# Performance work log

Hardware: AMD Instinct MI355X
Metric: run time of the kernel (lower is better)

The kernel has to match this reference:

```python
import jax, jax.numpy as jnp
import numpy as np


def setup_inputs() -> dict:
    key = jax.random.key(0)
    ks = jax.random.split(key, 10)
    B, T, D = 256, 256, 256
    CH, L, K = 128, 3, 10          # chunk_size, levels, conv_size
    H = CH * L                     # hidden_dim = 384
    G = 4 * H + 2 * L              # gate projection width = 1542
    HS = H // 6

    def xavier(k, shape):
        fan_in, fan_out = shape[0], shape[-1]
        lim = np.sqrt(6.0 / (fan_in + fan_out)).astype(np.float32)
        return jax.random.uniform(k, shape, jnp.float32, -lim, lim)

    x = jax.random.normal(ks[0], (B, T, D), jnp.float32)
    lengths = jax.random.randint(ks[1], (B,), 1, T + 1).astype(jnp.int64)
    Wk = xavier(ks[2], (D + 1, G)); bk = jnp.zeros((G,), jnp.float32)
    Wr = xavier(ks[3], (H + 1, G)); br = jnp.zeros((G,), jnp.float32)
    Ws = xavier(ks[4], (H, HS));    bs = jnp.zeros((HS,), jnp.float32)
    Wrs = xavier(ks[5], (HS, H));   brs = jnp.zeros((H,), jnp.float32)
    Wc = xavier(ks[6], (H, H, K)) / np.sqrt(K)  # Conv1d weight (out, in, k)
    bc = jnp.zeros((H,), jnp.float32)
    return {"x": x, "lengths": lengths, "Wk": Wk, "bk": bk, "Wr": Wr,
            "br": br, "Ws": Ws, "bs": bs, "Wrs": Wrs, "brs": brs,
            "Wc": Wc, "bc": bc}


def _cumax_l2r(z):
    return jnp.cumsum(jax.nn.softmax(z, axis=-1), axis=-1)


def _cumax_r2l(z):
    zf = jnp.flip(z, -1)
    return jnp.flip(jnp.cumsum(jax.nn.softmax(zf, axis=-1), axis=-1), -1)


def reference(x, lengths, Wk, bk, Wr, br, Ws, bs, Wrs, brs, Wc, bc):
    B, T, D = x.shape
    H = Wr.shape[0] - 1
    G = Wk.shape[1]
    L = (G - 4 * H) // 2
    CH = H // L
    K = Wc.shape[2]
    ones = jnp.ones((B, 1), x.dtype)

    def step(carry, xt):
        c, h, tmp_h, tmp_dis = carry
        # two linear projections (interval == 1 always)
        xo = (jnp.concatenate([xt, ones], -1) @ Wk + bk
              + jnp.concatenate([h, ones], -1) @ Wr + br)
        fm = _cumax_l2r(xo[:, :L])[:, :, None]          # (B,L,1)
        im = _cumax_r2l(xo[:, L:2 * L])[:, :, None]     # (B,L,1)
        rest = xo[:, 2 * L:].reshape(B, 4 * L, CH)
        f = jax.nn.sigmoid(rest[:, :L])
        i = jax.nn.sigmoid(rest[:, L:2 * L])
        o = jax.nn.sigmoid(rest[:, 2 * L:3 * L])
        c_in = jnp.tanh(rest[:, 3 * L:])
        c_last = c.reshape(B, L, CH)
        ov = fm * im
        c_new = (ov * (f * c_last + i * c_in)
                 + (fm - ov) * c_last + (im - ov) * c_in)
        h_new = (o * jnp.tanh(c_new)).reshape(B, H)
        c_new = c_new.reshape(B, H)
        cur_dis = 1.0 - jnp.mean(fm[..., 0], axis=-1)   # (B,)
        # sliding buffers (K, B, H) and (K, B)
        tmp_h = jnp.concatenate([tmp_h[1:], h_new[None]], 0)
        tmp_dis = jnp.concatenate([tmp_dis[1:], cur_dis[None]], 0)
        # local window attention weights
        ld = jax.nn.softmax(jnp.cumsum(tmp_dis.T, axis=1), axis=1)  # (B,K)
        local_h = tmp_h.transpose(1, 2, 0) * ld[:, None, :]         # (B,H,K)
        theme = jax.nn.sigmoid(
            jax.nn.relu(jnp.mean(local_h, -1) @ Ws + bs) @ Wrs + brs)
        conv = jnp.einsum('bhk,ohk->bo', local_h, Wc) + bc          # valid conv -> len 1
        local_out = theme * conv
        return (c_new, h_new, tmp_h, tmp_dis), (h_new, local_out)

    c0 = jnp.zeros((B, H), x.dtype)
    h0 = jnp.zeros((B, H), x.dtype)
    th0 = jnp.zeros((K, B, H), x.dtype)
    td0 = jnp.zeros((K, B), x.dtype)
    _, (origin_h, loc_h) = jax.lax.scan(step, (c0, h0, th0, td0),
                                        x.transpose(1, 0, 2))
    output = (loc_h + origin_h).transpose(1, 0, 2)   # (B,T,H)
    idx = jnp.clip(lengths, 1, T).astype(jnp.int32) - 1
    last_output = output[jnp.arange(B), idx]
    return (last_output, output)
```

## Files before the change

kernel.cpp:

```cpp
#include <hip/hip_runtime.h>
#include <hip/hip_bf16.h>
#include <cstddef>

#define B_  256
#define T_  256
#define D_  256
#define H_  384
#define G_  1542
#define L_  3
#define CH_ 128
#define K_  10
#define HS_ 64

#define NGRP 16
#define NMEM 16
#define GW   16
#define CPM  24
#define NFR  7
#define PCOLS 112
#define XOLP 114
#define NKC  20
#define W_LDS    (NKC * NFR * 64 * 8 * 2)
#define BIAS_OFF W_LDS
#define UNI_OFF  (W_LDS + 512)
#define HOUT_OFF 7296
#define SML_OFF  (HOUT_OFF + 768)
#define LDS_BYTES (UNI_OFF + SML_OFF + 256)

#define POST_LDS 153600

using bf16x8 = __attribute__((ext_vector_type(8))) short;
using f32x4  = __attribute__((ext_vector_type(4))) float;
typedef unsigned long long ull_t;

__device__ __forceinline__ float bf2f(unsigned short s) {
    return __uint_as_float(((unsigned)s) << 16);
}
__device__ __forceinline__ unsigned short f2bf(float f) {
    unsigned u = __float_as_uint(f);
    return (unsigned short)((u + 0x7fffu + ((u >> 16) & 1u)) >> 16);
}
__device__ __forceinline__ float sig_fast(float x) { return 1.f / (1.f + __expf(-x)); }
__device__ __forceinline__ float tanh_fast(float x) {
    float ax = fabsf(x);
    float t = __expf(-2.f * ax);
    float r = (1.f - t) / (1.f + t);
    return copysignf(r, x);
}

__device__ __forceinline__ int gcol_of(int member, int p) {
    if (p < 6) return p;
    if (p < 102) { int q = p - 6; return 6 + (q / CPM) * H_ + member * CPM + (q % CPM); }
    return -1;
}

__global__ __launch_bounds__(256)
void k_xa(const float* __restrict__ x, unsigned short* __restrict__ xA) {
    __shared__ float xl[64][261];
    const int t = blockIdx.x, bq = blockIdx.y;
    const int b0 = bq * 64, tid = threadIdx.x;
    for (int idx = tid; idx < 4096; idx += 256) {
        int row = idx >> 6, c4 = idx & 63;
        float4 v = *(const float4*)(x + ((size_t)(b0 + row) * T_ + t) * D_ + c4 * 4);
        xl[row][c4 * 4 + 0] = v.x; xl[row][c4 * 4 + 1] = v.y;
        xl[row][c4 * 4 + 2] = v.z; xl[row][c4 * 4 + 3] = v.w;
    }
    __syncthreads();
    for (int idx = tid; idx < 2048; idx += 256) {
        int lane = idx & 63, gl = (idx >> 6) & 3, kc = idx >> 8;
        int brow = gl * 16 + (lane & 15);
        int d = kc * 32 + (lane >> 4) * 8;
        unsigned o[4];
        #pragma unroll
        for (int q = 0; q < 4; ++q)
            o[q] = (unsigned)f2bf(xl[brow][d + 2 * q])
                 | ((unsigned)f2bf(xl[brow][d + 2 * q + 1]) << 16);
        int4 pk = make_int4((int)o[0], (int)o[1], (int)o[2], (int)o[3]);
        ((int4*)xA)[(((size_t)t * 8 + kc) * 16 + (bq * 4 + gl)) * 64 + lane] = pk;
    }
}

__global__ __launch_bounds__(256)
void k_prep(const float* __restrict__ Wk, const float* __restrict__ bk,
            const float* __restrict__ Wr, const float* __restrict__ br,
            const float* __restrict__ Ws, const float* __restrict__ Wrs,
            const float* __restrict__ Wc,
            unsigned short* __restrict__ Wf, unsigned short* __restrict__ Wg,
            unsigned short* __restrict__ WsT, unsigned short* __restrict__ WrsT,
            float* __restrict__ biasP, unsigned* __restrict__ flags)
{
    const int bid = blockIdx.x, tid = threadIdx.x;
    if (bid < 560) {
        int idx = bid * 256 + tid;
        int lane = idx & 63;
        int ni   = (idx >> 6) % NFR;
        int kc   = (idx / (64 * NFR)) % NKC;
        int member = idx / (64 * NFR * NKC);
        int p = ni * 16 + (lane & 15);
        int g = gcol_of(member, p);
        unsigned short out[8];
        #pragma unroll
        for (int j = 0; j < 8; ++j) {
            int k = kc * 32 + (lane >> 4) * 8 + j;
            float v = 0.f;
            if (g >= 0) v = (k < 256) ? Wk[(size_t)k * G_ + g] : Wr[(size_t)(k - 256) * G_ + g];
            out[j] = f2bf(v);
        }
        int4 pk;
        pk.x = (unsigned)out[0] | ((unsigned)out[1] << 16);
        pk.y = (unsigned)out[2] | ((unsigned)out[3] << 16);
        pk.z = (unsigned)out[4] | ((unsigned)out[5] << 16);
        pk.w = (unsigned)out[6] | ((unsigned)out[7] << 16);
        ((int4*)Wf)[idx] = pk;
    } else if (bid < 6320) {
        int idx = (bid - 560) * 256 + tid;
        int o = idx / (K_ * H_);
        int rem = idx % (K_ * H_);
        int k = rem / H_, h = rem % H_;
        Wg[idx] = f2bf(Wc[((size_t)o * H_ + h) * K_ + k]);
    } else if (bid < 6416) {
        int idx = (bid - 6320) * 256 + tid;
        int jj = idx / H_, k = idx % H_;
        WsT[idx] = f2bf(Ws[(size_t)k * HS_ + jj]);
    } else if (bid < 6512) {
        int idx = (bid - 6416) * 256 + tid;
        int o = idx / HS_, jj = idx % HS_;
        WrsT[idx] = f2bf(Wrs[(size_t)jj * H_ + o]);
    } else if (bid < 6519) {
        int idx = (bid - 6512) * 256 + tid;
        if (idx < NMEM * PCOLS) {
            int member = idx / PCOLS, p = idx % PCOLS;
            int g = gcol_of(member, p);
            biasP[idx] = (g >= 0)
                ? bk[g] + br[g] + Wk[(size_t)256 * G_ + g] + Wr[(size_t)384 * G_ + g] : 0.f;
        }
    } else {
        if (tid < NGRP * NMEM)
            __hip_atomic_store(flags + tid, 0u,
                               __ATOMIC_RELAXED, __HIP_MEMORY_SCOPE_AGENT);
    }
}

__global__ __launch_bounds__(512, 1)
void k_serial(const unsigned short* __restrict__ xA, const unsigned short* __restrict__ Wf,
              const float* __restrict__ biasP,
              unsigned short* __restrict__ hbf, float* __restrict__ dis,
              unsigned* __restrict__ flags)
{
    extern __shared__ char lds_raw[];
    unsigned short* Wl = (unsigned short*)lds_raw;
    float* biasL = (float*)(lds_raw + BIAS_OFF);
    char* uni = lds_raw + UNI_OFF;
    float* xol = (float*)uni;
    unsigned short* hout = (unsigned short*)(uni + HOUT_OFF);
    float* smL = (float*)(uni + SML_OFF);
    int4* stage4 = (int4*)uni;
    const bf16x8* stage = (const bf16x8*)uni;

    const int tid = threadIdx.x;
    const int lane = tid & 63, wave = tid >> 6;
    const int group = blockIdx.x & 15, member = blockIdx.x >> 4;
    const int b0 = group * GW;
    const int ni = wave;
    const bool domm = (wave < NFR);

    {
        const int4* src = (const int4*)(Wf + (size_t)member * (NKC * NFR * 64 * 8));
        for (int i = tid; i < W_LDS / 16; i += 512) ((int4*)Wl)[i] = src[i];
        if (tid < PCOLS) biasL[tid] = biasP[member * PCOLS + tid];
    }
    __syncthreads();

    const float bias_a = domm ? biasL[ni * 16 + (lane & 15)] : 0.f;

    const bool hasS = (tid < 384);
    const int skcl = tid >> 6, sln = tid & 63;
    const int st0 = skcl * 64 + sln;
    const unsigned short* src0 =
        hbf + (size_t)(b0 + (sln & 15)) * H_ + skcl * 32 + (sln >> 4) * 8;

    float c_r0 = 0.f;
    unsigned* gflags = flags + group * NMEM;

    for (int t = 0; t < T_; ++t) {
        bf16x8 xf[8];
        if (domm) {
            #pragma unroll
            for (int kc = 0; kc < 8; ++kc)
                xf[kc] = *((const bf16x8*)(xA
                    + (((size_t)t * 8 + kc) * 16 + group) * 512 + lane * 8));
        }

        if (t > 0) {
            if (tid < NMEM) {
                const unsigned tgt = (unsigned)t;
                while (__hip_atomic_load(gflags + tid, __ATOMIC_RELAXED,
                                         __HIP_MEMORY_SCOPE_AGENT) < tgt)
                    __builtin_amdgcn_s_sleep(1);
            }
            __syncthreads();
        }

        ull_t la0, la1, lb0, lb1;
        if (t > 0 && hasS) {
            const size_t toff = (size_t)(t - 1) * B_ * H_;
            const ull_t* p = (const ull_t*)(src0 + toff);
            la0 = __hip_atomic_load(p,     __ATOMIC_RELAXED, __HIP_MEMORY_SCOPE_AGENT);
            la1 = __hip_atomic_load(p + 1, __ATOMIC_RELAXED, __HIP_MEMORY_SCOPE_AGENT);
            p = (const ull_t*)(src0 + toff + 192);
            lb0 = __hip_atomic_load(p,     __ATOMIC_RELAXED, __HIP_MEMORY_SCOPE_AGENT);
            lb1 = __hip_atomic_load(p + 1, __ATOMIC_RELAXED, __HIP_MEMORY_SCOPE_AGENT);
        }

        f32x4 acc0 = f32x4{bias_a, bias_a, bias_a, bias_a};
        if (domm) {
            #pragma unroll
            for (int kc = 0; kc < 8; ++kc) {
                bf16x8 w0 = ((const bf16x8*)Wl)[(kc * NFR + ni) * 64 + lane];
                acc0 = __builtin_amdgcn_mfma_f32_16x16x32_bf16(xf[kc], w0, acc0, 0, 0, 0);
            }
        }

        if (t > 0) {
            if (hasS)
                stage4[st0] = make_int4((int)(la0 & 0xffffffffu), (int)(la0 >> 32),
                                        (int)(la1 & 0xffffffffu), (int)(la1 >> 32));
            __syncthreads();
            if (domm) {
                #pragma unroll
                for (int kcl = 0; kcl < 6; ++kcl) {
                    bf16x8 a0 = stage[kcl * 64 + lane];
                    bf16x8 w0 = ((const bf16x8*)Wl)[((8 + kcl) * NFR + ni) * 64 + lane];
                    acc0 = __builtin_amdgcn_mfma_f32_16x16x32_bf16(a0, w0, acc0, 0, 0, 0);
                }
            }
            __syncthreads();
            if (hasS)
                stage4[st0] = make_int4((int)(lb0 & 0xffffffffu), (int)(lb0 >> 32),
                                        (int)(lb1 & 0xffffffffu), (int)(lb1 >> 32));
            __syncthreads();
            if (domm) {
                #pragma unroll
                for (int kcl = 0; kcl < 6; ++kcl) {
                    bf16x8 a0 = stage[kcl * 64 + lane];
                    bf16x8 w0 = ((const bf16x8*)Wl)[((14 + kcl) * NFR + ni) * 64 + lane];
                    acc0 = __builtin_amdgcn_mfma_f32_16x16x32_bf16(a0, w0, acc0, 0, 0, 0);
                }
            }
        }
        __syncthreads();

        if (domm) {
            #pragma unroll
            for (int r = 0; r < 4; ++r)
                xol[((lane >> 4) * 4 + r) * XOLP + ni * 16 + (lane & 15)] = acc0[r];
        }
        __syncthreads();

        if (tid < GW) {
            const float* row = xol + tid * XOLP;
            float z0 = row[0], z1 = row[1], z2 = row[2];
            float z3 = row[3], z4 = row[4], z5 = row[5];
            float m1 = fmaxf(fmaxf(z0, z1), z2);
            float e0 = __expf(z0 - m1), e1 = __expf(z1 - m1), e2 = __expf(z2 - m1);
            float inv1 = 1.f / (e0 + e1 + e2);
            float fm0 = e0 * inv1, fm1 = (e0 + e1) * inv1;
            float m2 = fmaxf(fmaxf(z3, z4), z5);
            float f3 = __expf(z3 - m2), f4 = __expf(z4 - m2), f5 = __expf(z5 - m2);
            float inv2 = 1.f / (f3 + f4 + f5);
            smL[tid * 4 + 0] = fm0;
            smL[tid * 4 + 1] = fm1;
            smL[tid * 4 + 2] = (f4 + f5) * inv2;
            smL[tid * 4 + 3] = f5 * inv2;
            if (member == 0)
                dis[t * B_ + b0 + tid] = 1.f - (fm0 + fm1 + 1.f) * (1.f / 3.f);
        }
        __syncthreads();

        if (tid < 384) {
            int b = tid & 15, ch = tid >> 4;
            const float* row = xol + b * XOLP;
            float fm0 = smL[b * 4 + 0], fm1 = smL[b * 4 + 1];
            float im1 = smL[b * 4 + 2], im2 = smL[b * 4 + 3];

            int hh = member * CPM + ch;
            int l = hh >> 7;
            float fm = (l == 0) ? fm0 : (l == 1) ? fm1 : 1.f;
            float im = (l == 0) ? 1.f : (l == 1) ? im1 : im2;

            float fg = sig_fast(row[6 + ch]);
            float ig = sig_fast(row[6 + CPM + ch]);
            float og = sig_fast(row[6 + 2 * CPM + ch]);
            float ci = tanh_fast(row[6 + 3 * CPM + ch]);

            float ov = fm * im;
            float cn = ov * (fg * c_r0 + ig * ci) + (fm - ov) * c_r0 + (im - ov) * ci;
            float hn = og * tanh_fast(cn);
            c_r0 = cn;

            hout[b * CPM + ch] = f2bf(hn);
        }
        __syncthreads();

        if (tid < 96) {
            int b = tid / 6, jj = tid % 6;
            ull_t v = *(const ull_t*)&hout[b * CPM + jj * 4];
            __hip_atomic_store(
                (ull_t*)(hbf + ((size_t)t * B_ + b0 + b) * H_ + member * CPM + jj * 4),
                v, __ATOMIC_RELAXED, __HIP_MEMORY_SCOPE_AGENT);
        }
        __syncthreads();

        if (tid == 0)
            __hip_atomic_store(gflags + member, (unsigned)(t + 1),
                               __ATOMIC_RELAXED, __HIP_MEMORY_SCOPE_AGENT);
    }
}

__global__ __launch_bounds__(512, 1)
void k_post(const unsigned short* __restrict__ hbf, const float* __restrict__ dis,
            const unsigned short* __restrict__ Wg,
            const unsigned short* __restrict__ WsT, const unsigned short* __restrict__ WrsT,
            const float* __restrict__ bs, const float* __restrict__ brs,
            const float* __restrict__ bc, float* __restrict__ out_part)
{
    extern __shared__ char plds[];
    float* ldl = (float*)plds;
    unsigned short* AlB = (unsigned short*)(plds + 10240);
    unsigned short* BlB = (unsigned short*)(plds + 92160);
    unsigned short* hbarL = (unsigned short*)(plds + 10240);
    unsigned short* uL = (unsigned short*)(plds + 65536);

    const int b0 = blockIdx.x * 64;
    const int t0 = blockIdx.y * 4;
    const int tid = threadIdx.x;
    const int wave = tid >> 6, lane = tid & 63;
    const int mh = wave >> 2, nq = wave & 3;

    if (tid < 256) {
        int ti = tid >> 6, bi = tid & 63;
        int t = t0 + ti, b = b0 + bi;
        float s = 0.f, sk[K_];
        #pragma unroll
        for (int k = 0; k < K_; ++k) {
            int tau = t - (K_ - 1) + k;
            float d = (tau >= 0) ? dis[tau * B_ + b] : 0.f;
            s += d; sk[k] = s;
        }
        float m = sk[0];
        #pragma unroll
        for (int k = 1; k < K_; ++k) m = fmaxf(m, sk[k]);
        float sum = 0.f;
        #pragma unroll
        for (int k = 0; k < K_; ++k) { sk[k] = __expf(sk[k] - m); sum += sk[k]; }
        float inv = 1.f / sum;
        #pragma unroll
        for (int k = 0; k < K_; ++k) ldl[ti * 640 + bi * 10 + k] = sk[k] * inv;
    }

    auto loadA = [&](int ch, int4 av[2], bool valid[2]) {
        int k = ch / 12, hb = (ch % 12) * 32;
        #pragma unroll
        for (int i = 0; i < 2; ++i) {
            int s = tid + 512 * i;
            int ti = s >> 8, rem = s & 255;
            int bb = rem >> 2, half = rem & 3;
            int tau = t0 + ti - (K_ - 1) + k;
            valid[i] = (tau >= 0);
            if (valid[i])
                av[i] = *(const int4*)(hbf + ((size_t)tau * B_ + b0 + bb) * H_ + hb + half * 8);
        }
    };
    auto loadB = [&](int ch, int4 bv[3]) {
        #pragma unroll
        for (int q = 0; q < 3; ++q) {
            int idx = q * 512 + tid;
            int row = idx >> 2, half = idx & 3;
            bv[q] = *(const int4*)(Wg + (size_t)row * 3840 + ch * 32 + half * 8);
        }
    };
    auto writeA = [&](int buf, int ch, const int4 av[2], const bool valid[2]) {
        int k = ch / 12;
        #pragma unroll
        for (int i = 0; i < 2; ++i) {
            int s = tid + 512 * i;
            int ti = s >> 8, rem = s & 255;
            int bb = rem >> 2, half = rem & 3;
            int4 pk = make_int4(0, 0, 0, 0);
            if (valid[i]) {
                float l = ldl[ti * 640 + bb * 10 + k];
                unsigned vv[4] = {(unsigned)av[i].x, (unsigned)av[i].y,
                                  (unsigned)av[i].z, (unsigned)av[i].w};
                unsigned o[4];
                #pragma unroll
                for (int q = 0; q < 4; ++q) {
                    float flo = __uint_as_float(vv[q] << 16) * l;
                    float fhi = __uint_as_float(vv[q] & 0xffff0000u) * l;
                    o[q] = (unsigned)f2bf(flo) | ((unsigned)f2bf(fhi) << 16);
                }
                pk = make_int4((int)o[0], (int)o[1], (int)o[2], (int)o[3]);
            }
            *(int4*)&AlB[buf * 10240 + ti * 2560 + bb * 40 + half * 8] = pk;
        }
    };
    auto writeB = [&](int buf, const int4 bv[3]) {
        #pragma unroll
        for (int q = 0; q < 3; ++q) {
            int idx = q * 512 + tid;
            int row = idx >> 2, half = idx & 3;
            *(int4*)&BlB[buf * 15360 + row * 40 + half * 8] = bv[q];
        }
    };

    int4 av[2]; bool avalid[2]; int4 bv[3];
    loadA(0, av, avalid); loadB(0, bv);
    __syncthreads();
    writeA(0, 0, av, avalid); writeB(0, bv);

    f32x4 acc[4][2][6] = {};
    for (int ch = 0; ch < 120; ++ch) {
        int cur = ch & 1;
        bool more = (ch + 1 < 120);
        if (more) { loadA(ch + 1, av, avalid); loadB(ch + 1, bv); }
        __syncthreads();
        if (more) { writeA(cur ^ 1, ch + 1, av, avalid); writeB(cur ^ 1, bv); }

        bf16x8 af[4][2];
        #pragma unroll
        for (int ti = 0; ti < 4; ++ti)
            #pragma unroll
            for (int mi = 0; mi < 2; ++mi)
                af[ti][mi] = *(const bf16x8*)&AlB[cur * 10240 + ti * 2560
                    + (mh * 32 + mi * 16 + (lane & 15)) * 40 + (lane >> 4) * 8];
        #pragma unroll
        for (int ni = 0; ni < 6; ++ni) {
            bf16x8 bfv = *(const bf16x8*)&BlB[cur * 15360
                + (nq * 96 + ni * 16 + (lane & 15)) * 40 + (lane >> 4) * 8];
            #pragma unroll
            for (int ti = 0; ti < 4; ++ti)
                #pragma unroll
                for (int mi = 0; mi < 2; ++mi)
                    acc[ti][mi][ni] = __builtin_amdgcn_mfma_f32_16x16x32_bf16(
                        af[ti][mi], bfv, acc[ti][mi][ni], 0, 0, 0);
        }
    }
    __syncthreads();

    #pragma unroll
    for (int ti = 0; ti < 4; ++ti) {
        const int t = t0 + ti;
        for (int idx = tid; idx < 3072; idx += 512) {
            int bb = idx / 48, h8 = idx % 48;
            float s[8] = {};
            #pragma unroll
            for (int k = 0; k < K_; ++k) {
                int tau = t - (K_ - 1) + k;
                if (tau >= 0) {
                    int4 v = *(const int4*)(hbf + ((size_t)tau * B_ + b0 + bb) * H_ + h8 * 8);
                    float l = ldl[ti * 640 + bb * 10 + k];
                    unsigned vv[4] = {(unsigned)v.x, (unsigned)v.y, (unsigned)v.z, (unsigned)v.w};
                    #pragma unroll
                    for (int q = 0; q < 4; ++q) {
                        s[2 * q]     = fmaf(__uint_as_float(vv[q] << 16), l, s[2 * q]);
                        s[2 * q + 1] = fmaf(__uint_as_float(vv[q] & 0xffff0000u), l, s[2 * q + 1]);
                    }
                }
            }
            unsigned o[4];
            #pragma unroll
            for (int q = 0; q < 4; ++q)
                o[q] = (unsigned)f2bf(s[2 * q] * 0.1f) | ((unsigned)f2bf(s[2 * q + 1] * 0.1f) << 16);
            *(int4*)&hbarL[bb * 400 + h8 * 8] = make_int4((int)o[0], (int)o[1], (int)o[2], (int)o[3]);
        }
        __syncthreads();

        if (wave < 4) {
            f32x4 uacc[4] = {};
            for (int kc = 0; kc < 12; ++kc) {
                bf16x8 a = *(const bf16x8*)&hbarL[(wave * 16 + (lane & 15)) * 400
                                                  + kc * 32 + (lane >> 4) * 8];
                #pragma unroll
                for (int ni = 0; ni < 4; ++ni) {
                    bf16x8 wb = *(const bf16x8*)(WsT + (size_t)(ni * 16 + (lane & 15)) * H_
                                                 + kc * 32 + (lane >> 4) * 8);
                    uacc[ni] = __builtin_amdgcn_mfma_f32_16x16x32_bf16(a, wb, uacc[ni], 0, 0, 0);
                }
            }
            #pragma unroll
            for (int ni = 0; ni < 4; ++ni) {
                float bsv = bs[ni * 16 + (lane & 15)];
                #pragma unroll
                for (int r = 0; r < 4; ++r)
                    uL[(wave * 16 + (lane >> 4) * 4 + r) * 72 + ni * 16 + (lane & 15)] =
                        f2bf(fmaxf(uacc[ni][r] + bsv, 0.f));
            }
        }
        __syncthreads();

        #pragma unroll
        for (int half = 0; half < 2; ++half) {
            f32x4 tacc[2][3] = {};
            #pragma unroll
            for (int kc = 0; kc < 2; ++kc) {
                bf16x8 ua[2];
                #pragma unroll
                for (int mi = 0; mi < 2; ++mi)
                    ua[mi] = *(const bf16x8*)&uL[(mh * 32 + mi * 16 + (lane & 15)) * 72
                                                 + kc * 32 + (lane >> 4) * 8];
                #pragma unroll
                for (int n3 = 0; n3 < 3; ++n3) {
                    int ni = half * 3 + n3;
                    bf16x8 wb = *(const bf16x8*)(WrsT
                        + (size_t)(nq * 96 + ni * 16 + (lane & 15)) * HS_
                        + kc * 32 + (lane >> 4) * 8);
                    #pragma unroll
                    for (int mi = 0; mi < 2; ++mi)
                        tacc[mi][n3] = __builtin_amdgcn_mfma_f32_16x16x32_bf16(
                            ua[mi], wb, tacc[mi][n3], 0, 0, 0);
                }
            }
            #pragma unroll
            for (int mi = 0; mi < 2; ++mi) {
                #pragma unroll
                for (int n3 = 0; n3 < 3; ++n3) {
                    int ni = half * 3 + n3;
                    int o = nq * 96 + ni * 16 + (lane & 15);
                    float brsv = brs[o], bcv = bc[o];
                    int brow0 = b0 + mh * 32 + mi * 16 + ((lane >> 4) << 2);
                    #pragma unroll
                    for (int r = 0; r < 4; ++r) {
                        float th = sig_fast(tacc[mi][n3][r] + brsv);
                        float cv = acc[ti][mi][ni][r] + bcv;
                        float hv = bf2f(hbf[((size_t)t * B_ + brow0 + r) * H_ + o]);
                        out_part[((size_t)(brow0 + r) * T_ + t) * H_ + o] = hv + th * cv;
                    }
                }
            }
        }
        __syncthreads();
    }
}

__global__ void k_last(const int* __restrict__ len_i, const float* __restrict__ out_part,
                       float* __restrict__ last)
{
    int b = blockIdx.x, tid = threadIdx.x;
    bool is64 = (len_i[1] == 0);
    long long v = is64 ? ((const long long*)len_i)[b] : (long long)len_i[b];
    int idx = (int)v;
    idx = max(1, min(T_, idx)) - 1;
    last[(size_t)b * H_ + tid] = out_part[((size_t)b * T_ + idx) * H_ + tid];
}

extern "C" void kernel_launch(void* const* d_in, const int* in_sizes, int n_in,
                              void* d_out, int out_size, void* d_ws, size_t ws_size,
                              hipStream_t stream) {
    const float* x   = (const float*)d_in[0];
    const int*   len = (const int*)d_in[1];
    const float* Wk  = (const float*)d_in[2];
    const float* bk  = (const float*)d_in[3];
    const float* Wr  = (const float*)d_in[4];
    const float* br  = (const float*)d_in[5];
    const float* Ws  = (const float*)d_in[6];
    const float* bs  = (const float*)d_in[7];
    const float* Wrs = (const float*)d_in[8];
    const float* brs = (const float*)d_in[9];
    const float* Wc  = (const float*)d_in[10];
    const float* bc  = (const float*)d_in[11];

    float* out      = (float*)d_out;
    float* last     = out;
    float* out_part = out + (size_t)B_ * H_;

    char* p = (char*)d_ws;
    unsigned*       flags  = (unsigned*)p;       p += 1024;
    float*          dis    = (float*)p;          p += (size_t)T_ * B_ * 4;
    unsigned short* xA     = (unsigned short*)p; p += (size_t)T_ * B_ * D_ * 2;
    unsigned short* WfragG = (unsigned short*)p; p += (size_t)NMEM * NKC * NFR * 64 * 8 * 2;
    float*          biasP  = (float*)p;          p += (size_t)NMEM * PCOLS * 4;
    unsigned short* hbf    = (unsigned short*)p; p += (size_t)T_ * B_ * H_ * 2;
    unsigned short* Wg     = (unsigned short*)p; p += (size_t)H_ * K_ * H_ * 2;
    unsigned short* WsT    = (unsigned short*)p; p += (size_t)HS_ * H_ * 2;
    unsigned short* WrsT   = (unsigned short*)p; p += (size_t)H_ * HS_ * 2;

    k_xa  <<<dim3(T_, 4), 256, 0, stream>>>(x, xA);
    k_prep<<<6520, 256, 0, stream>>>(Wk, bk, Wr, br, Ws, Wrs, Wc,
                                     WfragG, Wg, WsT, WrsT, biasP, flags);

    hipFuncSetAttribute((const void*)k_serial,
                        hipFuncAttributeMaxDynamicSharedMemorySize, LDS_BYTES);
    hipFuncSetAttribute((const void*)k_post,
                        hipFuncAttributeMaxDynamicSharedMemorySize, POST_LDS);

    k_serial<<<NGRP * NMEM, 512, LDS_BYTES, stream>>>(xA, WfragG, biasP, hbf, dis, flags);
    k_post <<<dim3(4, 64), 512, POST_LDS, stream>>>(hbf, dis, Wg, WsT, WrsT, bs, brs, bc, out_part);
    k_last <<<B_, H_, 0, stream>>>(len, out_part, last);
}
```

Before: 1.478 ms.

## Replace per-step flag barrier with sentinel-polled hidden-state data in serial LSTM

The cross-block flag handshake is removed. The hidden-state buffer is pre-filled with an all-ones sentinel, and each consumer spins on the data words themselves until they are no longer the sentinel, so one flag round-trip and several block barriers per timestep disappear. The two-stage h staging is merged into a single 12-chunk LDS stage, and the small-softmax step is fused into the per-channel threads to drop an extra barrier. The cost is a large sentinel fill of hbf in the prep kernel, plus redundant softmax work across threads. It also relies on a real bf16 quad never equalling the sentinel bit pattern.

```diff
diff --git a/kernel.cpp b/kernel.cpp
--- a/kernel.cpp
+++ b/kernel.cpp
@@ -23,11 +23,12 @@
 #define W_LDS    (NKC * NFR * 64 * 8 * 2)
 #define BIAS_OFF W_LDS
 #define UNI_OFF  (W_LDS + 512)
-#define HOUT_OFF 7296
-#define SML_OFF  (HOUT_OFF + 768)
-#define LDS_BYTES (UNI_OFF + SML_OFF + 256)
+#define HOUT_OFF 12288
+#define LDS_BYTES (UNI_OFF + HOUT_OFF + 768)
 
 #define POST_LDS 153600
+
+#define SENT 0xFFFFFFFFFFFFFFFFull
 
 using bf16x8 = __attribute__((ext_vector_type(8))) short;
 using f32x4  = __attribute__((ext_vector_type(4))) float;
@@ -46,6 +47,9 @@
     float t = __expf(-2.f * ax);
     float r = (1.f - t) / (1.f + t);
     return copysignf(r, x);
+}
+__device__ __forceinline__ ull_t ldA(const ull_t* p) {
+    return __hip_atomic_load(p, __ATOMIC_RELAXED, __HIP_MEMORY_SCOPE_AGENT);
 }
 
 __device__ __forceinline__ int gcol_of(int member, int p) {
@@ -85,13 +89,20 @@
             const float* __restrict__ Wr, const float* __restrict__ br,
             const float* __restrict__ Ws, const float* __restrict__ Wrs,
             const float* __restrict__ Wc,
-            unsigned short* __restrict__ Wf, unsigned short* __restrict__ Wg,
-            unsigned short* __restrict__ WsT, unsigned short* __restrict__ WrsT,
-            float* __restrict__ biasP, unsigned* __restrict__ flags)
+            unsigned short* __restrict__ hbf, unsigned short* __restrict__ Wf,
+            unsigned short* __restrict__ Wg, unsigned short* __restrict__ WsT,
+            unsigned short* __restrict__ WrsT, float* __restrict__ biasP)
 {
     const int bid = blockIdx.x, tid = threadIdx.x;
-    if (bid < 560) {
-        int idx = bid * 256 + tid;
+    if (bid < 2048) {
+        ull_t* hb = (ull_t*)hbf;
+        int base = bid * 256 + tid;
+        #pragma unroll
+        for (int j = 0; j < 12; ++j)
+            __hip_atomic_store(hb + base + j * 524288, SENT,
+                               __ATOMIC_RELAXED, __HIP_MEMORY_SCOPE_AGENT);
+    } else if (bid < 2608) {
+        int idx = (bid - 2048) * 256 + tid;
         int lane = idx & 63;
         int ni   = (idx >> 6) % NFR;
         int kc   = (idx / (64 * NFR)) % NKC;
@@ -112,40 +123,35 @@
         pk.z = (unsigned)out[4] | ((unsigned)out[5] << 16);
         pk.w = (unsigned)out[6] | ((unsigned)out[7] << 16);
         ((int4*)Wf)[idx] = pk;
-    } else if (bid < 6320) {
-        int idx = (bid - 560) * 256 + tid;
+    } else if (bid < 8368) {
+        int idx = (bid - 2608) * 256 + tid;
         int o = idx / (K_ * H_);
         int rem = idx % (K_ * H_);
         int k = rem / H_, h = rem % H_;
         Wg[idx] = f2bf(Wc[((size_t)o * H_ + h) * K_ + k]);
-    } else if (bid < 6416) {
-        int idx = (bid - 6320) * 256 + tid;
+    } else if (bid < 8464) {
+        int idx = (bid - 8368) * 256 + tid;
         int jj = idx / H_, k = idx % H_;
         WsT[idx] = f2bf(Ws[(size_t)k * HS_ + jj]);
-    } else if (bid < 6512) {
-        int idx = (bid - 6416) * 256 + tid;
+    } else if (bid < 8560) {
+        int idx = (bid - 8464) * 256 + tid;
         int o = idx / HS_, jj = idx % HS_;
         WrsT[idx] = f2bf(Wrs[(size_t)jj * H_ + o]);
-    } else if (bid < 6519) {
-        int idx = (bid - 6512) * 256 + tid;
+    } else {
+        int idx = (bid - 8560) * 256 + tid;
         if (idx < NMEM * PCOLS) {
             int member = idx / PCOLS, p = idx % PCOLS;
             int g = gcol_of(member, p);
             biasP[idx] = (g >= 0)
                 ? bk[g] + br[g] + Wk[(size_t)256 * G_ + g] + Wr[(size_t)384 * G_ + g] : 0.f;
         }
-    } else {
-        if (tid < NGRP * NMEM)
-            __hip_atomic_store(flags + tid, 0u,
-                               __ATOMIC_RELAXED, __HIP_MEMORY_SCOPE_AGENT);
     }
 }
 
 __global__ __launch_bounds__(512, 1)
 void k_serial(const unsigned short* __restrict__ xA, const unsigned short* __restrict__ Wf,
               const float* __restrict__ biasP,
-              unsigned short* __restrict__ hbf, float* __restrict__ dis,
-              unsigned* __restrict__ flags)
+              unsigned short* __restrict__ hbf, float* __restrict__ dis)
 {
     extern __shared__ char lds_raw[];
     unsigned short* Wl = (unsigned short*)lds_raw;
@@ -153,7 +159,6 @@
     char* uni = lds_raw + UNI_OFF;
     float* xol = (float*)uni;
     unsigned short* hout = (unsigned short*)(uni + HOUT_OFF);
-    float* smL = (float*)(uni + SML_OFF);
     int4* stage4 = (int4*)uni;
     const bf16x8* stage = (const bf16x8*)uni;
 
@@ -175,12 +180,12 @@
 
     const bool hasS = (tid < 384);
     const int skcl = tid >> 6, sln = tid & 63;
-    const int st0 = skcl * 64 + sln;
+    const int stA = skcl * 64 + sln;
+    const int stB = (skcl + 6) * 64 + sln;
     const unsigned short* src0 =
         hbf + (size_t)(b0 + (sln & 15)) * H_ + skcl * 32 + (sln >> 4) * 8;
 
     float c_r0 = 0.f;
-    unsigned* gflags = flags + group * NMEM;
 
     for (int t = 0; t < T_; ++t) {
         bf16x8 xf[8];
@@ -191,64 +196,51 @@
                     + (((size_t)t * 8 + kc) * 16 + group) * 512 + lane * 8));
         }
 
+        f32x4 acc0 = f32x4{bias_a, bias_a, bias_a, bias_a};
+
         if (t > 0) {
-            if (tid < NMEM) {
-                const unsigned tgt = (unsigned)t;
-                while (__hip_atomic_load(gflags + tid, __ATOMIC_RELAXED,
-                                         __HIP_MEMORY_SCOPE_AGENT) < tgt)
-                    __builtin_amdgcn_s_sleep(1);
-            }
-            __syncthreads();
-        }
-
-        ull_t la0, la1, lb0, lb1;
-        if (t > 0 && hasS) {
             const size_t toff = (size_t)(t - 1) * B_ * H_;
-            const ull_t* p = (const ull_t*)(src0 + toff);
-            la0 = __hip_atomic_load(p,     __ATOMIC_RELAXED, __HIP_MEMORY_SCOPE_AGENT);
-            la1 = __hip_atomic_load(p + 1, __ATOMIC_RELAXED, __HIP_MEMORY_SCOPE_AGENT);
-            p = (const ull_t*)(src0 + toff + 192);
-            lb0 = __hip_atomic_load(p,     __ATOMIC_RELAXED, __HIP_MEMORY_SCOPE_AGENT);
-            lb1 = __hip_atomic_load(p + 1, __ATOMIC_RELAXED, __HIP_MEMORY_SCOPE_AGENT);
-        }
-
-        f32x4 acc0 = f32x4{bias_a, bias_a, bias_a, bias_a};
-        if (domm) {
-            #pragma unroll
-            for (int kc = 0; kc < 8; ++kc) {
-                bf16x8 w0 = ((const bf16x8*)Wl)[(kc * NFR + ni) * 64 + lane];
-                acc0 = __builtin_amdgcn_mfma_f32_16x16x32_bf16(xf[kc], w0, acc0, 0, 0, 0);
-            }
-        }
-
-        if (t > 0) {
-            if (hasS)
-                stage4[st0] = make_int4((int)(la0 & 0xffffffffu), (int)(la0 >> 32),
-                                        (int)(la1 & 0xffffffffu), (int)(la1 >> 32));
+            const ull_t* pA = (const ull_t*)(src0 + toff);
+            const ull_t* pB = (const ull_t*)(src0 + toff + 192);
+            ull_t v0 = 0, v1 = 0, v2 = 0, v3 = 0;
+            if (hasS) { v0 = ldA(pA); v1 = ldA(pA + 1); v2 = ldA(pB); v3 = ldA(pB + 1); }
+
+            if (domm) {
+                #pragma unroll
+                for (int kc = 0; kc < 8; ++kc) {
+                    bf16x8 w0 = ((const bf16x8*)Wl)[(kc * NFR + ni) * 64 + lane];
+                    acc0 = __builtin_amdgcn_mfma_f32_16x16x32_bf16(xf[kc], w0, acc0, 0, 0, 0);
+                }
+            }
+
+            if (hasS) {
+                while ((v0 == SENT) || (v1 == SENT) || (v2 == SENT) || (v3 == SENT)) {
+                    v0 = ldA(pA); v1 = ldA(pA + 1); v2 = ldA(pB); v3 = ldA(pB + 1);
+                }
+                stage4[stA] = make_int4((int)(v0 & 0xffffffffu), (int)(v0 >> 32),
+                                        (int)(v1 & 0xffffffffu), (int)(v1 >> 32));
+                stage4[stB] = make_int4((int)(v2 & 0xffffffffu), (int)(v2 >> 32),
+                                        (int)(v3 & 0xffffffffu), (int)(v3 >> 32));
+            }
             __syncthreads();
             if (domm) {
                 #pragma unroll
-                for (int kcl = 0; kcl < 6; ++kcl) {
+                for (int kcl = 0; kcl < 12; ++kcl) {
                     bf16x8 a0 = stage[kcl * 64 + lane];
                     bf16x8 w0 = ((const bf16x8*)Wl)[((8 + kcl) * NFR + ni) * 64 + lane];
                     acc0 = __builtin_amdgcn_mfma_f32_16x16x32_bf16(a0, w0, acc0, 0, 0, 0);
                 }
             }
             __syncthreads();
-            if (hasS)
-                stage4[st0] = make_int4((int)(lb0 & 0xffffffffu), (int)(lb0 >> 32),
-                                        (int)(lb1 & 0xffffffffu), (int)(lb1 >> 32));
-            __syncthreads();
+        } else {
             if (domm) {
                 #pragma unroll
-                for (int kcl = 0; kcl < 6; ++kcl) {
-                    bf16x8 a0 = stage[kcl * 64 + lane];
-                    bf16x8 w0 = ((const bf16x8*)Wl)[((14 + kcl) * NFR + ni) * 64 + lane];
-                    acc0 = __builtin_amdgcn_mfma_f32_16x16x32_bf16(a0, w0, acc0, 0, 0, 0);
-                }
-            }
-        }
-        __syncthreads();
+                for (int kc = 0; kc < 8; ++kc) {
+                    bf16x8 w0 = ((const bf16x8*)Wl)[(kc * NFR + ni) * 64 + lane];
+                    acc0 = __builtin_amdgcn_mfma_f32_16x16x32_bf16(xf[kc], w0, acc0, 0, 0, 0);
+                }
+            }
+        }
 
         if (domm) {
             #pragma unroll
@@ -257,8 +249,9 @@
         }
         __syncthreads();
 
-        if (tid < GW) {
-            const float* row = xol + tid * XOLP;
+        if (tid < 384) {
+            int b = tid & 15, ch = tid >> 4;
+            const float* row = xol + b * XOLP;
             float z0 = row[0], z1 = row[1], z2 = row[2];
             float z3 = row[3], z4 = row[4], z5 = row[5];
             float m1 = fmaxf(fmaxf(z0, z1), z2);
@@ -268,20 +261,7 @@
             float m2 = fmaxf(fmaxf(z3, z4), z5);
             float f3 = __expf(z3 - m2), f4 = __expf(z4 - m2), f5 = __expf(z5 - m2);
             float inv2 = 1.f / (f3 + f4 + f5);
-            smL[tid * 4 + 0] = fm0;
-            smL[tid * 4 + 1] = fm1;
-            smL[tid * 4 + 2] = (f4 + f5) * inv2;
-            smL[tid * 4 + 3] = f5 * inv2;
-            if (member == 0)
-                dis[t * B_ + b0 + tid] = 1.f - (fm0 + fm1 + 1.f) * (1.f / 3.f);
-        }
-        __syncthreads();
-
-        if (tid < 384) {
-            int b = tid & 15, ch = tid >> 4;
-            const float* row = xol + b * XOLP;
-            float fm0 = smL[b * 4 + 0], fm1 = smL[b * 4 + 1];
-            float im1 = smL[b * 4 + 2], im2 = smL[b * 4 + 3];
+            float im1 = (f4 + f5) * inv2, im2 = f5 * inv2;
 
             int hh = member * CPM + ch;
             int l = hh >> 7;
@@ -299,6 +279,8 @@
             c_r0 = cn;
 
             hout[b * CPM + ch] = f2bf(hn);
+            if (member == 0 && ch == 0)
+                dis[t * B_ + b0 + b] = 1.f - (fm0 + fm1 + 1.f) * (1.f / 3.f);
         }
         __syncthreads();
 
@@ -309,11 +291,6 @@
                 (ull_t*)(hbf + ((size_t)t * B_ + b0 + b) * H_ + member * CPM + jj * 4),
                 v, __ATOMIC_RELAXED, __HIP_MEMORY_SCOPE_AGENT);
         }
-        __syncthreads();
-
-        if (tid == 0)
-            __hip_atomic_store(gflags + member, (unsigned)(t + 1),
-                               __ATOMIC_RELAXED, __HIP_MEMORY_SCOPE_AGENT);
     }
 }
 
@@ -573,7 +550,6 @@
     float* out_part = out + (size_t)B_ * H_;
 
     char* p = (char*)d_ws;
-    unsigned*       flags  = (unsigned*)p;       p += 1024;
     float*          dis    = (float*)p;          p += (size_t)T_ * B_ * 4;
     unsigned short* xA     = (unsigned short*)p; p += (size_t)T_ * B_ * D_ * 2;
     unsigned short* WfragG = (unsigned short*)p; p += (size_t)NMEM * NKC * NFR * 64 * 8 * 2;
@@ -584,15 +560,15 @@
     unsigned short* WrsT   = (unsigned short*)p; p += (size_t)H_ * HS_ * 2;
 
     k_xa  <<<dim3(T_, 4), 256, 0, stream>>>(x, xA);
-    k_prep<<<6520, 256, 0, stream>>>(Wk, bk, Wr, br, Ws, Wrs, Wc,
-                                     WfragG, Wg, WsT, WrsT, biasP, flags);
+    k_prep<<<8567, 256, 0, stream>>>(Wk, bk, Wr, br, Ws, Wrs, Wc,
+                                     hbf, WfragG, Wg, WsT, WrsT, biasP);
 
     hipFuncSetAttribute((const void*)k_serial,
                         hipFuncAttributeMaxDynamicSharedMemorySize, LDS_BYTES);
     hipFuncSetAttribute((const void*)k_post,
                         hipFuncAttributeMaxDynamicSharedMemorySize, POST_LDS);
 
-    k_serial<<<NGRP * NMEM, 512, LDS_BYTES, stream>>>(xA, WfragG, biasP, hbf, dis, flags);
+    k_serial<<<NGRP * NMEM, 512, LDS_BYTES, stream>>>(xA, WfragG, biasP, hbf, dis);
     k_post <<<dim3(4, 64), 512, POST_LDS, stream>>>(hbf, dis, Wg, WsT, WrsT, bs, brs, bc, out_part);
     k_last <<<B_, H_, 0, stream>>>(len, out_part, last);
 }
```

Result: faster. 1.383 ms (-6.4%).
